# Performance work log

Hardware: AMD Instinct MI355X
Metric: run time of the kernel (lower is better)

The kernel has to match this reference:

```python
import jax, jax.numpy as jnp
import numpy as np

N_NODES = 50000
N_EDGES = 1600000
IN_DIM = 128
HID = 64
N_GRAPHS = 256


def gcn_conv(x, row, col, W, b, n_nodes):
    """PyG GCNConv: symmetric gcn_norm with self-loops, linear-then-aggregate."""
    h = x @ W  # [N, out]
    loop = jnp.arange(n_nodes, dtype=row.dtype)
    r = jnp.concatenate([row, loop])  # sources (messages from x[r])
    c = jnp.concatenate([col, loop])  # targets (aggregate at c)
    ew = jnp.ones(r.shape[0], dtype=x.dtype)
    deg = jax.ops.segment_sum(ew, c, num_segments=n_nodes)
    dinv = jnp.where(deg > 0, jax.lax.rsqrt(deg), 0.0).astype(x.dtype)
    norm = dinv[r] * dinv[c]  # [E+N]
    out = jax.ops.segment_sum(norm[:, None] * h[r], c, num_segments=n_nodes)
    return out + b


def global_mean_pool(x, batch, n_graphs):
    sums = jax.ops.segment_sum(x, batch, num_segments=n_graphs)
    cnt = jax.ops.segment_sum(jnp.ones(x.shape[0], x.dtype), batch, num_segments=n_graphs)
    return sums / jnp.clip(cnt, 1.0)[:, None]


def setup_inputs() -> dict:
    key = jax.random.key(0)
    ks = jax.random.split(key, 12)
    x = jax.random.normal(ks[0], (N_NODES, IN_DIM), dtype=jnp.float32)
    edge_index = jax.random.randint(ks[1], (2, N_EDGES), 0, N_NODES, dtype=jnp.int64)
    batch = jnp.sort(jax.random.randint(ks[2], (N_NODES,), 0, N_GRAPHS, dtype=jnp.int64))
    def glorot(k, shp):
        lim = float(np.sqrt(6.0 / (shp[0] + shp[1])))
        return jax.random.uniform(k, shp, jnp.float32, -lim, lim)
    return {
        "x": x,
        "edge_index": edge_index,
        "batch": batch,
        "W1": glorot(ks[3], (IN_DIM, HID)), "b1": jnp.zeros((HID,), jnp.float32),
        "W2": glorot(ks[4], (HID, HID)), "b2": jnp.zeros((HID,), jnp.float32),
        "W3": glorot(ks[5], (HID, HID)), "b3": jnp.zeros((HID,), jnp.float32),
        "Wl1": glorot(ks[6], (HID, 16)), "bl1": jnp.zeros((16,), jnp.float32),
        "Wl2": glorot(ks[7], (16, 1)), "bl2": jnp.zeros((1,), jnp.float32),
    }


def reference(x, edge_index, batch, W1, b1, W2, b2, W3, b3, Wl1, bl1, Wl2, bl2):
    n = x.shape[0]
    row, col = edge_index[0], edge_index[1]
    h = jax.nn.relu(gcn_conv(x, row, col, W1, b1, n))
    h = jax.nn.relu(gcn_conv(h, row, col, W2, b2, n))
    h = jax.nn.relu(gcn_conv(h, row, col, W3, b3, n))
    g = global_mean_pool(h, batch, N_GRAPHS)  # [G, 64]
    out = (g @ Wl1 + bl1) @ Wl2 + bl2  # [G, 1]
    return out
```

## Files before the change

kernel.cpp:

```cpp
#include <hip/hip_runtime.h>

#define HID 64
#define B1 256
#define NBMAX 200
#define CAP 10368

typedef __attribute__((ext_vector_type(8))) short short8;
typedef __attribute__((ext_vector_type(4))) float float4v;

__device__ __forceinline__ ushort f2bf(float f) {
  unsigned u = __float_as_uint(f);
  unsigned r = (u + 0x7fffu + ((u >> 16) & 1u)) >> 16;
  return (ushort)r;
}
__device__ __forceinline__ float bf2f(ushort v) {
  return __uint_as_float(((unsigned)v) << 16);
}
__device__ __forceinline__ float4 up4(ushort4 v) {
  float4 r;
  r.x = bf2f(v.x);
  r.y = bf2f(v.y);
  r.z = bf2f(v.z);
  r.w = bf2f(v.w);
  return r;
}


__global__ __launch_bounds__(256) void bucket_hist(const int* __restrict__ col, int E, int epb,
                                                   int* __restrict__ buckettot,
                                                   const float* __restrict__ W1,
                                                   const float* __restrict__ W2,
                                                   const float* __restrict__ W3,
                                                   ushort* __restrict__ Wt1h, ushort* __restrict__ Wt1l,
                                                   ushort* __restrict__ Wt2h, ushort* __restrict__ Wt2l,
                                                   ushort* __restrict__ Wt3h, ushort* __restrict__ Wt3l) {
  int b = blockIdx.x, t = threadIdx.x;
  int gt = b * 256 + t;
  if (gt < 128 * 64) {
    int k = gt >> 6, nn = gt & 63;
    float w = W1[gt];
    ushort h = f2bf(w);
    Wt1h[nn * 128 + k] = h;
    Wt1l[nn * 128 + k] = f2bf(w - bf2f(h));
  }
  if (gt < 64 * 64) {
    int k = gt >> 6, nn = gt & 63;
    float w2 = W2[gt], w3 = W3[gt];
    ushort h2 = f2bf(w2), h3 = f2bf(w3);
    Wt2h[nn * 64 + k] = h2;
    Wt2l[nn * 64 + k] = f2bf(w2 - bf2f(h2));
    Wt3h[nn * 64 + k] = h3;
    Wt3l[nn * 64 + k] = f2bf(w3 - bf2f(h3));
  }

  __shared__ int cnt[256];
  cnt[t] = 0;
  __syncthreads();
  int lo = b * epb, hi = min(lo + epb, E);
  for (int e = lo + t; e < hi; e += 256) atomicAdd(&cnt[col[e] >> 8], 1);
  __syncthreads();
  int v = cnt[t];
  if (v > 0) atomicAdd(&buckettot[t], v);
}

__global__ __launch_bounds__(256) void scan_buckettot(const int* __restrict__ buckettot,
                                                      int* __restrict__ bucketbase,
                                                      int* __restrict__ woffglob,
                                                      int* __restrict__ csr_off, int n, int E,
                                                      int nb) {
  __shared__ int s[256];
  int t = threadIdx.x;
  int v = (t < nb) ? buckettot[t] : 0;
  s[t] = v;
  __syncthreads();
  for (int d = 1; d < 256; d <<= 1) {
    int u = (t >= d) ? s[t - d] : 0;
    __syncthreads();
    s[t] += u;
    __syncthreads();
  }
  int base = (t == 0) ? 0 : s[t - 1];
  if (t <= nb) bucketbase[t] = base;
  woffglob[t] = base;
  if (t == 0) csr_off[n] = E;
}

__global__ __launch_bounds__(256) void bin_edges(const int* __restrict__ row,
                                                 const int* __restrict__ col, int E, int epb,
                                                 int* __restrict__ woffglob,
                                                 unsigned* __restrict__ binned) {
  __shared__ int cnt[256];
  __shared__ int ofs[256];
  __shared__ int gb[256];
  __shared__ int lcur[256];
  __shared__ unsigned stage[4096];
  int b = blockIdx.x, t = threadIdx.x;
  int lo = b * epb, hi = min(lo + epb, E);

  for (int bs = lo; bs < hi; bs += 4096) {
    int ecnt = min(4096, hi - bs);
    cnt[t] = 0;
    __syncthreads();
    for (int i = t; i < ecnt; i += 256) atomicAdd(&cnt[col[bs + i] >> 8], 1);
    __syncthreads();
    int v = cnt[t];
    ofs[t] = v;
    __syncthreads();
    for (int d = 1; d < 256; d <<= 1) {
      int u = (t >= d) ? ofs[t - d] : 0;
      __syncthreads();
      ofs[t] += u;
      __syncthreads();
    }
    int excl = ofs[t] - v;
    int g = 0;
    if (v > 0) g = atomicAdd(&woffglob[t], v);
    __syncthreads();
    ofs[t] = excl;
    gb[t] = g;
    lcur[t] = excl;
    __syncthreads();
    for (int i = t; i < ecnt; i += 256) {
      int c = col[bs + i];
      int r = row[bs + i];
      int p = atomicAdd(&lcur[c >> 8], 1);
      stage[p] = ((unsigned)r << 16) | (unsigned)c;
    }
    __syncthreads();
    for (int i = t; i < ecnt; i += 256) {
      unsigned en = stage[i];
      int bb = (en >> 8) & 255;
      binned[gb[bb] + (i - ofs[bb])] = en;
    }
    __syncthreads();
  }
}

__global__ __launch_bounds__(256) void bucket_csr(const unsigned* __restrict__ binned,
                                                  const int* __restrict__ bucketbase,
                                                  int* __restrict__ csr_off,
                                                  int* __restrict__ csr_src,
                                                  float* __restrict__ dinv, int n) {
  __shared__ int lcnt[256];
  __shared__ int lofs[256];
  __shared__ int lsrc[CAP];
  int k = blockIdx.x, t = threadIdx.x;
  int base = bucketbase[k], end = bucketbase[k + 1];
  int s = end - base;
  lcnt[t] = 0;
  __syncthreads();
  for (int i = t; i < s; i += 256) {
    unsigned p = binned[base + i];
    atomicAdd(&lcnt[p & 255u], 1);
  }
  __syncthreads();
  int v = lcnt[t];
  lofs[t] = v;
  __syncthreads();
  for (int d = 1; d < 256; d <<= 1) {
    int u = (t >= d) ? lofs[t - d] : 0;
    __syncthreads();
    lofs[t] += u;
    __syncthreads();
  }
  int excl = lofs[t] - v;
  int node = (k << 8) + t;
  if (node < n) {
    csr_off[node] = base + excl;
    dinv[node] = rsqrtf((float)(v + 1));
  }
  lcnt[t] = excl;
  __syncthreads();
  for (int i = t; i < s; i += 256) {
    unsigned p = binned[base + i];
    int pos = atomicAdd(&lcnt[p & 255u], 1);
    if (pos < CAP) lsrc[pos] = (int)(p >> 16);
  }
  __syncthreads();
  for (int i = t; i < s; i += 256) csr_src[base + i] = (i < CAP) ? lsrc[i] : 0;
}


template <int K>
__global__ __launch_bounds__(256) void gemm_mfma(const float* __restrict__ A,
                                                 const ushort* __restrict__ Wh,
                                                 const ushort* __restrict__ Wl,
                                                 const float* __restrict__ dinv,
                                                 ushort* __restrict__ out, int n) {
  int wave = (blockIdx.x * 256 + threadIdx.x) >> 6;
  int lane = threadIdx.x & 63;
  int row0 = wave * 16;
  if (row0 >= n) return;
  int m = lane & 15;
  int quad = lane >> 4;
  int r = row0 + m;
  int rc = (r < n) ? r : (n - 1);

  float4v acc[4];
#pragma unroll
  for (int t = 0; t < 4; ++t) acc[t] = (float4v){0.f, 0.f, 0.f, 0.f};

#pragma unroll
  for (int k0 = 0; k0 < K; k0 += 32) {
    const float4* xp = (const float4*)&A[(size_t)rc * K + k0 + quad * 8];
    float4 a0 = xp[0];
    float4 a1 = xp[1];
    float av[8] = {a0.x, a0.y, a0.z, a0.w, a1.x, a1.y, a1.z, a1.w};
    short8 ah, al;
#pragma unroll
    for (int i = 0; i < 8; ++i) {
      ushort h = f2bf(av[i]);
      ah[i] = (short)h;
      al[i] = (short)f2bf(av[i] - bf2f(h));
    }
#pragma unroll
    for (int t = 0; t < 4; ++t) {
      size_t wof = (size_t)(t * 16 + m) * K + k0 + quad * 8;
      short8 bh = *(const short8*)&Wh[wof];
      short8 bl = *(const short8*)&Wl[wof];
      acc[t] = __builtin_amdgcn_mfma_f32_16x16x32_bf16(ah, bh, acc[t], 0, 0, 0);
      acc[t] = __builtin_amdgcn_mfma_f32_16x16x32_bf16(al, bh, acc[t], 0, 0, 0);
      acc[t] = __builtin_amdgcn_mfma_f32_16x16x32_bf16(ah, bl, acc[t], 0, 0, 0);
    }
  }

  float4 dv = ((const float4*)dinv)[(row0 >> 2) + quad];
  float dvi[4] = {dv.x, dv.y, dv.z, dv.w};
#pragma unroll
  for (int i = 0; i < 4; ++i) {
    int orow = row0 + quad * 4 + i;
    if (orow < n) {
#pragma unroll
      for (int t = 0; t < 4; ++t) {
        out[(size_t)orow * 64 + t * 16 + m] = f2bf(dvi[i] * acc[t][i]);
      }
    }
  }
}


__global__ __launch_bounds__(256) void agg_kernel(
    const ushort* __restrict__ hs, const int* __restrict__ csr_off,
    const int* __restrict__ csr_src, const float* __restrict__ dinv,
    const float* __restrict__ bias, float* __restrict__ out, int n) {
  int wid = (blockIdx.x * 256 + threadIdx.x) >> 6;
  int lane = threadIdx.x & 63;
  if (wid >= n) return;
  int qe = lane >> 4;
  int fq = lane & 15;
  const ushort4* hs4 = (const ushort4*)hs;

  float4 acc = make_float4(0.f, 0.f, 0.f, 0.f);
  if (qe == 0) {
    float4 s = up4(hs4[(size_t)wid * 16 + fq]);
    acc.x += s.x; acc.y += s.y; acc.z += s.z; acc.w += s.w;
  }

  int j = csr_off[wid];
  int e = csr_off[wid + 1];

  int pre = min(e, (j + 3) & ~3);
  if (j + qe < pre) {
    int s0 = csr_src[j + qe];
    float4 f = up4(hs4[(size_t)s0 * 16 + fq]);
    acc.x += f.x; acc.y += f.y; acc.z += f.z; acc.w += f.w;
  }
  int base = pre;

  for (; base + 16 <= e; base += 16) {
    int4 s = *(const int4*)&csr_src[base + qe * 4];
    float4 f0 = up4(hs4[(size_t)s.x * 16 + fq]);
    float4 f1 = up4(hs4[(size_t)s.y * 16 + fq]);
    float4 f2 = up4(hs4[(size_t)s.z * 16 + fq]);
    float4 f3 = up4(hs4[(size_t)s.w * 16 + fq]);
    acc.x += f0.x + f1.x + f2.x + f3.x;
    acc.y += f0.y + f1.y + f2.y + f3.y;
    acc.z += f0.z + f1.z + f2.z + f3.z;
    acc.w += f0.w + f1.w + f2.w + f3.w;
  }

  for (; base + 4 <= e; base += 4) {
    int s0 = csr_src[base + qe];
    float4 f = up4(hs4[(size_t)s0 * 16 + fq]);
    acc.x += f.x; acc.y += f.y; acc.z += f.z; acc.w += f.w;
  }
  if (base + qe < e) {
    int s0 = csr_src[base + qe];
    float4 f = up4(hs4[(size_t)s0 * 16 + fq]);
    acc.x += f.x; acc.y += f.y; acc.z += f.z; acc.w += f.w;
  }

  acc.x += __shfl_xor(acc.x, 16, 64);
  acc.y += __shfl_xor(acc.y, 16, 64);
  acc.z += __shfl_xor(acc.z, 16, 64);
  acc.w += __shfl_xor(acc.w, 16, 64);
  acc.x += __shfl_xor(acc.x, 32, 64);
  acc.y += __shfl_xor(acc.y, 32, 64);
  acc.z += __shfl_xor(acc.z, 32, 64);
  acc.w += __shfl_xor(acc.w, 32, 64);

  if (qe == 0) {
    float d = dinv[wid];
    float4 bi = ((const float4*)bias)[fq];
    float4 r;
    r.x = fmaxf(d * acc.x + bi.x, 0.f);
    r.y = fmaxf(d * acc.y + bi.y, 0.f);
    r.z = fmaxf(d * acc.z + bi.z, 0.f);
    r.w = fmaxf(d * acc.w + bi.w, 0.f);
    ((float4*)out)[(size_t)wid * 16 + fq] = r;
  }
}


__global__ __launch_bounds__(256) void pool_mlp_kernel(
    const float* __restrict__ a, const int* __restrict__ batch, int n,
    const float* __restrict__ Wl1, const float* __restrict__ bl1,
    const float* __restrict__ Wl2, const float* __restrict__ bl2,
    float* __restrict__ out) {
  int g = blockIdx.x;
  int t = threadIdx.x;
  int lane = t & 63;
  int w = t >> 6;

  int lo = 0, hi = n;
  while (lo < hi) {
    int m = (lo + hi) >> 1;
    if (batch[m] < g) lo = m + 1; else hi = m;
  }
  int start = lo;
  lo = start; hi = n;
  while (lo < hi) {
    int m = (lo + hi) >> 1;
    if (batch[m] < g + 1) lo = m + 1; else hi = m;
  }
  int end = lo;

  float s = 0.f;
  for (int i = start + w; i < end; i += 4) s += a[i * 64 + lane];

  __shared__ float ps[4][64];
  __shared__ float gv[64];
  __shared__ float hv[16];
  ps[w][lane] = s;
  __syncthreads();
  if (w == 0) {
    float tot = ps[0][lane] + ps[1][lane] + ps[2][lane] + ps[3][lane];
    gv[lane] = tot / (float)max(end - start, 1);
  }
  __syncthreads();
  if (t < 16) {
    float h = bl1[t];
    for (int k = 0; k < 64; ++k) h += gv[k] * Wl1[k * 16 + t];
    hv[t] = h;
  }
  __syncthreads();
  if (t == 0) {
    float o = bl2[0];
    for (int j2 = 0; j2 < 16; ++j2) o += hv[j2] * Wl2[j2];
    out[g] = o;
  }
}


extern "C" void kernel_launch(void* const* d_in, const int* in_sizes, int n_in,
                              void* d_out, int out_size, void* d_ws, size_t ws_size,
                              hipStream_t stream) {
  const float* x = (const float*)d_in[0];
  const int* ei = (const int*)d_in[1];
  const int* batch = (const int*)d_in[2];
  const float* W1 = (const float*)d_in[3];
  const float* b1 = (const float*)d_in[4];
  const float* W2 = (const float*)d_in[5];
  const float* b2 = (const float*)d_in[6];
  const float* W3 = (const float*)d_in[7];
  const float* b3 = (const float*)d_in[8];
  const float* Wl1 = (const float*)d_in[9];
  const float* bl1 = (const float*)d_in[10];
  const float* Wl2 = (const float*)d_in[11];
  const float* bl2 = (const float*)d_in[12];

  int n = in_sizes[0] / 128;
  int E = in_sizes[1] / 2;
  int G = out_size;
  int nb = (n + 255) >> 8;
  int epb = (E + B1 - 1) / B1;

  const int* row = ei;
  const int* col = ei + E;

  char* p = (char*)d_ws;
  int* buckettot = (int*)p;   p += 256 * 4;
  int* bucketbase = (int*)p;  p += 272 * 4;
  int* woffglob = (int*)p;    p += 256 * 4;
  int* csr_off = (int*)p;     p += 50064 * 4;
  float* dinv = (float*)p;    p += 50016 * 4;
  ushort* Wt1h = (ushort*)p;  p += 128 * 64 * 2;
  ushort* Wt1l = (ushort*)p;  p += 128 * 64 * 2;
  ushort* Wt2h = (ushort*)p;  p += 64 * 64 * 2;
  ushort* Wt2l = (ushort*)p;  p += 64 * 64 * 2;
  ushort* Wt3h = (ushort*)p;  p += 64 * 64 * 2;
  ushort* Wt3l = (ushort*)p;  p += 64 * 64 * 2;
  int* csr_src = (int*)p;     p += (size_t)((E + 15) / 16 * 16) * 4;
  ushort* hs = (ushort*)p;    p += (size_t)n * 64 * 2;
  float* abuf = (float*)p;
  unsigned* binned = (unsigned*)hs;

  hipMemsetAsync(buckettot, 0, 256 * 4, stream);
  bucket_hist<<<B1, 256, 0, stream>>>(col, E, epb, buckettot,
                                      W1, W2, W3, Wt1h, Wt1l, Wt2h, Wt2l, Wt3h, Wt3l);
  scan_buckettot<<<1, 256, 0, stream>>>(buckettot, bucketbase, woffglob, csr_off, n, E, nb);
  bin_edges<<<B1, 256, 0, stream>>>(row, col, E, epb, woffglob, binned);
  bucket_csr<<<nb, 256, 0, stream>>>(binned, bucketbase, csr_off, csr_src, dinv, n);

  int nwaves = (n + 15) / 16;
  int gblocks = (nwaves + 3) / 4;
  int ablocks = (n * 64 + 255) / 256;

  gemm_mfma<128><<<gblocks, 256, 0, stream>>>(x, Wt1h, Wt1l, dinv, hs, n);
  agg_kernel<<<ablocks, 256, 0, stream>>>(hs, csr_off, csr_src, dinv, b1, abuf, n);
  gemm_mfma<64><<<gblocks, 256, 0, stream>>>(abuf, Wt2h, Wt2l, dinv, hs, n);
  agg_kernel<<<ablocks, 256, 0, stream>>>(hs, csr_off, csr_src, dinv, b2, abuf, n);
  gemm_mfma<64><<<gblocks, 256, 0, stream>>>(abuf, Wt3h, Wt3l, dinv, hs, n);
  agg_kernel<<<ablocks, 256, 0, stream>>>(hs, csr_off, csr_src, dinv, b3, abuf, n);
  pool_mlp_kernel<<<G, 256, 0, stream>>>(abuf, batch, n, Wl1, bl1, Wl2, bl2, (float*)d_out);
}
```

Before: 332.1 us.

## Fuse aggregation with next-layer GEMM and fold mean-pool into final aggregation

Aggregation of layers 1 and 2 now runs inside one kernel with the following MFMA GEMM. Each wave gathers 16 nodes into shared memory, then multiplies them by the next weight matrix, so the fp32 activation buffer no longer goes through global memory. The last aggregation atomically adds into per-graph sums, which replaces the separate pool pass. The bucket histogram writes per-block counts that one kernel then reduces, which removes a memset and the global atomics. In exchange, one wave now handles 16 nodes one after another, which lowers parallelism in the gather phase, and float atomics into 256 graph rows may contend.

```diff
diff --git a/kernel.cpp b/kernel.cpp
--- a/kernel.cpp
+++ b/kernel.cpp
@@ -1,9 +1,7 @@
 #include <hip/hip_runtime.h>
 
-#define HID 64
 #define B1 256
-#define NBMAX 200
-#define CAP 10368
+#define CAP 8960
 
 typedef __attribute__((ext_vector_type(8))) short short8;
 typedef __attribute__((ext_vector_type(4))) float float4v;
@@ -26,16 +24,18 @@
 }
 
 
-__global__ __launch_bounds__(256) void bucket_hist(const int* __restrict__ col, int E, int epb,
-                                                   int* __restrict__ buckettot,
-                                                   const float* __restrict__ W1,
-                                                   const float* __restrict__ W2,
-                                                   const float* __restrict__ W3,
-                                                   ushort* __restrict__ Wt1h, ushort* __restrict__ Wt1l,
-                                                   ushort* __restrict__ Wt2h, ushort* __restrict__ Wt2l,
-                                                   ushort* __restrict__ Wt3h, ushort* __restrict__ Wt3l) {
+__global__ __launch_bounds__(256) void hist_prep(const int* __restrict__ col, int E, int epb,
+                                                 int* __restrict__ blockcnt,
+                                                 float* __restrict__ gsum,
+                                                 const float* __restrict__ W1,
+                                                 const float* __restrict__ W2,
+                                                 const float* __restrict__ W3,
+                                                 ushort* __restrict__ Wt1h, ushort* __restrict__ Wt1l,
+                                                 ushort* __restrict__ Wt2h, ushort* __restrict__ Wt2l,
+                                                 ushort* __restrict__ Wt3h, ushort* __restrict__ Wt3l) {
   int b = blockIdx.x, t = threadIdx.x;
   int gt = b * 256 + t;
+  if (gt < 256 * 64) gsum[gt] = 0.f;
   if (gt < 128 * 64) {
     int k = gt >> 6, nn = gt & 63;
     float w = W1[gt];
@@ -59,18 +59,18 @@
   int lo = b * epb, hi = min(lo + epb, E);
   for (int e = lo + t; e < hi; e += 256) atomicAdd(&cnt[col[e] >> 8], 1);
   __syncthreads();
-  int v = cnt[t];
-  if (v > 0) atomicAdd(&buckettot[t], v);
-}
-
-__global__ __launch_bounds__(256) void scan_buckettot(const int* __restrict__ buckettot,
-                                                      int* __restrict__ bucketbase,
-                                                      int* __restrict__ woffglob,
-                                                      int* __restrict__ csr_off, int n, int E,
-                                                      int nb) {
+  blockcnt[b * 256 + t] = cnt[t];
+}
+
+
+__global__ __launch_bounds__(256) void megascan(const int* __restrict__ blockcnt,
+                                                int* __restrict__ bucketbase,
+                                                int* __restrict__ woffglob,
+                                                int* __restrict__ csr_off, int n, int E, int nb) {
   __shared__ int s[256];
   int t = threadIdx.x;
-  int v = (t < nb) ? buckettot[t] : 0;
+  int v = 0;
+  for (int b = 0; b < 256; ++b) v += blockcnt[b * 256 + t];
   s[t] = v;
   __syncthreads();
   for (int d = 1; d < 256; d <<= 1) {
@@ -84,6 +84,7 @@
   woffglob[t] = base;
   if (t == 0) csr_off[n] = E;
 }
+
 
 __global__ __launch_bounds__(256) void bin_edges(const int* __restrict__ row,
                                                  const int* __restrict__ col, int E, int epb,
@@ -123,8 +124,8 @@
     for (int i = t; i < ecnt; i += 256) {
       int c = col[bs + i];
       int r = row[bs + i];
-      int p = atomicAdd(&lcur[c >> 8], 1);
-      stage[p] = ((unsigned)r << 16) | (unsigned)c;
+      int pos = atomicAdd(&lcur[c >> 8], 1);
+      stage[pos] = ((unsigned)r << 16) | (unsigned)c;
     }
     __syncthreads();
     for (int i = t; i < ecnt; i += 256) {
@@ -135,6 +136,7 @@
     __syncthreads();
   }
 }
+
 
 __global__ __launch_bounds__(256) void bucket_csr(const unsigned* __restrict__ binned,
                                                   const int* __restrict__ bucketbase,
@@ -239,10 +241,144 @@
 }
 
 
-__global__ __launch_bounds__(256) void agg_kernel(
+__global__ __launch_bounds__(256) void layer_fused(
+    const ushort* __restrict__ hsIn, const int* __restrict__ csr_off,
+    const int* __restrict__ csr_src, const float* __restrict__ dinv,
+    const float* __restrict__ bias, const ushort* __restrict__ Wh,
+    const ushort* __restrict__ Wl, ushort* __restrict__ hsOut, int n) {
+  __shared__ float stage[4][16][76];
+  int w = threadIdx.x >> 6;
+  int lane = threadIdx.x & 63;
+  int tile = (blockIdx.x * 256 + threadIdx.x) >> 6;
+  int ntiles = (n + 15) >> 4;
+  if (tile >= ntiles) return;
+  int qe = lane >> 4;
+  int fq = lane & 15;
+  const ushort4* hs4 = (const ushort4*)hsIn;
+
+  for (int m = 0; m < 16; ++m) {
+    int wid = tile * 16 + m;
+    float4 acc = make_float4(0.f, 0.f, 0.f, 0.f);
+    float d = 0.f;
+    if (wid < n) {
+      d = dinv[wid];
+      if (qe == 0) acc = up4(hs4[(size_t)wid * 16 + fq]);
+      int j = csr_off[wid];
+      int e = csr_off[wid + 1];
+      int pre = min(e, (j + 3) & ~3);
+      if (j + qe < pre) {
+        int s0 = csr_src[j + qe];
+        float4 f = up4(hs4[(size_t)s0 * 16 + fq]);
+        acc.x += f.x; acc.y += f.y; acc.z += f.z; acc.w += f.w;
+      }
+      int base = pre;
+      for (; base + 32 <= e; base += 32) {
+        int4 sa = *(const int4*)&csr_src[base + qe * 4];
+        int4 sb = *(const int4*)&csr_src[base + 16 + qe * 4];
+        float4 f0 = up4(hs4[(size_t)sa.x * 16 + fq]);
+        float4 f1 = up4(hs4[(size_t)sa.y * 16 + fq]);
+        float4 f2 = up4(hs4[(size_t)sa.z * 16 + fq]);
+        float4 f3 = up4(hs4[(size_t)sa.w * 16 + fq]);
+        float4 f4 = up4(hs4[(size_t)sb.x * 16 + fq]);
+        float4 f5 = up4(hs4[(size_t)sb.y * 16 + fq]);
+        float4 f6 = up4(hs4[(size_t)sb.z * 16 + fq]);
+        float4 f7 = up4(hs4[(size_t)sb.w * 16 + fq]);
+        acc.x += (f0.x + f1.x) + (f2.x + f3.x) + ((f4.x + f5.x) + (f6.x + f7.x));
+        acc.y += (f0.y + f1.y) + (f2.y + f3.y) + ((f4.y + f5.y) + (f6.y + f7.y));
+        acc.z += (f0.z + f1.z) + (f2.z + f3.z) + ((f4.z + f5.z) + (f6.z + f7.z));
+        acc.w += (f0.w + f1.w) + (f2.w + f3.w) + ((f4.w + f5.w) + (f6.w + f7.w));
+      }
+      for (; base + 16 <= e; base += 16) {
+        int4 s = *(const int4*)&csr_src[base + qe * 4];
+        float4 f0 = up4(hs4[(size_t)s.x * 16 + fq]);
+        float4 f1 = up4(hs4[(size_t)s.y * 16 + fq]);
+        float4 f2 = up4(hs4[(size_t)s.z * 16 + fq]);
+        float4 f3 = up4(hs4[(size_t)s.w * 16 + fq]);
+        acc.x += f0.x + f1.x + f2.x + f3.x;
+        acc.y += f0.y + f1.y + f2.y + f3.y;
+        acc.z += f0.z + f1.z + f2.z + f3.z;
+        acc.w += f0.w + f1.w + f2.w + f3.w;
+      }
+      for (; base + 4 <= e; base += 4) {
+        int s0 = csr_src[base + qe];
+        float4 f = up4(hs4[(size_t)s0 * 16 + fq]);
+        acc.x += f.x; acc.y += f.y; acc.z += f.z; acc.w += f.w;
+      }
+      if (base + qe < e) {
+        int s0 = csr_src[base + qe];
+        float4 f = up4(hs4[(size_t)s0 * 16 + fq]);
+        acc.x += f.x; acc.y += f.y; acc.z += f.z; acc.w += f.w;
+      }
+      acc.x += __shfl_xor(acc.x, 16, 64);
+      acc.y += __shfl_xor(acc.y, 16, 64);
+      acc.z += __shfl_xor(acc.z, 16, 64);
+      acc.w += __shfl_xor(acc.w, 16, 64);
+      acc.x += __shfl_xor(acc.x, 32, 64);
+      acc.y += __shfl_xor(acc.y, 32, 64);
+      acc.z += __shfl_xor(acc.z, 32, 64);
+      acc.w += __shfl_xor(acc.w, 32, 64);
+    }
+    if (qe == 0) {
+      float4 bi = ((const float4*)bias)[fq];
+      float4 r;
+      r.x = fmaxf(d * acc.x + bi.x, 0.f);
+      r.y = fmaxf(d * acc.y + bi.y, 0.f);
+      r.z = fmaxf(d * acc.z + bi.z, 0.f);
+      r.w = fmaxf(d * acc.w + bi.w, 0.f);
+      *(float4*)&stage[w][m][fq * 4] = r;
+    }
+  }
+
+  int m2 = lane & 15;
+  int quad = lane >> 4;
+  float4v acc2[4];
+#pragma unroll
+  for (int t = 0; t < 4; ++t) acc2[t] = (float4v){0.f, 0.f, 0.f, 0.f};
+
+#pragma unroll
+  for (int k0 = 0; k0 < 64; k0 += 32) {
+    float4 a0 = *(const float4*)&stage[w][m2][k0 + quad * 8];
+    float4 a1 = *(const float4*)&stage[w][m2][k0 + quad * 8 + 4];
+    float av[8] = {a0.x, a0.y, a0.z, a0.w, a1.x, a1.y, a1.z, a1.w};
+    short8 ah, al;
+#pragma unroll
+    for (int i = 0; i < 8; ++i) {
+      ushort h = f2bf(av[i]);
+      ah[i] = (short)h;
+      al[i] = (short)f2bf(av[i] - bf2f(h));
+    }
+#pragma unroll
+    for (int t = 0; t < 4; ++t) {
+      size_t wof = (size_t)(t * 16 + m2) * 64 + k0 + quad * 8;
+      short8 bh = *(const short8*)&Wh[wof];
+      short8 bl = *(const short8*)&Wl[wof];
+      acc2[t] = __builtin_amdgcn_mfma_f32_16x16x32_bf16(ah, bh, acc2[t], 0, 0, 0);
+      acc2[t] = __builtin_amdgcn_mfma_f32_16x16x32_bf16(al, bh, acc2[t], 0, 0, 0);
+      acc2[t] = __builtin_amdgcn_mfma_f32_16x16x32_bf16(ah, bl, acc2[t], 0, 0, 0);
+    }
+  }
+
+  int row0 = tile * 16;
+  float4 dv = ((const float4*)dinv)[(row0 >> 2) + quad];
+  float dvi[4] = {dv.x, dv.y, dv.z, dv.w};
+#pragma unroll
+  for (int i = 0; i < 4; ++i) {
+    int orow = row0 + quad * 4 + i;
+    if (orow < n) {
+#pragma unroll
+      for (int t = 0; t < 4; ++t) {
+        hsOut[(size_t)orow * 64 + t * 16 + m2] = f2bf(dvi[i] * acc2[t][i]);
+      }
+    }
+  }
+}
+
+
+__global__ __launch_bounds__(256) void agg_final(
     const ushort* __restrict__ hs, const int* __restrict__ csr_off,
     const int* __restrict__ csr_src, const float* __restrict__ dinv,
-    const float* __restrict__ bias, float* __restrict__ out, int n) {
+    const float* __restrict__ bias, const int* __restrict__ batch,
+    float* __restrict__ gsum, int n) {
   int wid = (blockIdx.x * 256 + threadIdx.x) >> 6;
   int lane = threadIdx.x & 63;
   if (wid >= n) return;
@@ -251,14 +387,10 @@
   const ushort4* hs4 = (const ushort4*)hs;
 
   float4 acc = make_float4(0.f, 0.f, 0.f, 0.f);
-  if (qe == 0) {
-    float4 s = up4(hs4[(size_t)wid * 16 + fq]);
-    acc.x += s.x; acc.y += s.y; acc.z += s.z; acc.w += s.w;
-  }
+  if (qe == 0) acc = up4(hs4[(size_t)wid * 16 + fq]);
 
   int j = csr_off[wid];
   int e = csr_off[wid + 1];
-
   int pre = min(e, (j + 3) & ~3);
   if (j + qe < pre) {
     int s0 = csr_src[j + qe];
@@ -266,7 +398,22 @@
     acc.x += f.x; acc.y += f.y; acc.z += f.z; acc.w += f.w;
   }
   int base = pre;
-
+  for (; base + 32 <= e; base += 32) {
+    int4 sa = *(const int4*)&csr_src[base + qe * 4];
+    int4 sb = *(const int4*)&csr_src[base + 16 + qe * 4];
+    float4 f0 = up4(hs4[(size_t)sa.x * 16 + fq]);
+    float4 f1 = up4(hs4[(size_t)sa.y * 16 + fq]);
+    float4 f2 = up4(hs4[(size_t)sa.z * 16 + fq]);
+    float4 f3 = up4(hs4[(size_t)sa.w * 16 + fq]);
+    float4 f4 = up4(hs4[(size_t)sb.x * 16 + fq]);
+    float4 f5 = up4(hs4[(size_t)sb.y * 16 + fq]);
+    float4 f6 = up4(hs4[(size_t)sb.z * 16 + fq]);
+    float4 f7 = up4(hs4[(size_t)sb.w * 16 + fq]);
+    acc.x += (f0.x + f1.x) + (f2.x + f3.x) + ((f4.x + f5.x) + (f6.x + f7.x));
+    acc.y += (f0.y + f1.y) + (f2.y + f3.y) + ((f4.y + f5.y) + (f6.y + f7.y));
+    acc.z += (f0.z + f1.z) + (f2.z + f3.z) + ((f4.z + f5.z) + (f6.z + f7.z));
+    acc.w += (f0.w + f1.w) + (f2.w + f3.w) + ((f4.w + f5.w) + (f6.w + f7.w));
+  }
   for (; base + 16 <= e; base += 16) {
     int4 s = *(const int4*)&csr_src[base + qe * 4];
     float4 f0 = up4(hs4[(size_t)s.x * 16 + fq]);
@@ -278,7 +425,6 @@
     acc.z += f0.z + f1.z + f2.z + f3.z;
     acc.w += f0.w + f1.w + f2.w + f3.w;
   }
-
   for (; base + 4 <= e; base += 4) {
     int s0 = csr_src[base + qe];
     float4 f = up4(hs4[(size_t)s0 * 16 + fq]);
@@ -307,20 +453,23 @@
     r.y = fmaxf(d * acc.y + bi.y, 0.f);
     r.z = fmaxf(d * acc.z + bi.z, 0.f);
     r.w = fmaxf(d * acc.w + bi.w, 0.f);
-    ((float4*)out)[(size_t)wid * 16 + fq] = r;
-  }
-}
-
-
-__global__ __launch_bounds__(256) void pool_mlp_kernel(
-    const float* __restrict__ a, const int* __restrict__ batch, int n,
+    int g = batch[wid];
+    float* gp = &gsum[(size_t)g * 64 + fq * 4];
+    atomicAdd(gp + 0, r.x);
+    atomicAdd(gp + 1, r.y);
+    atomicAdd(gp + 2, r.z);
+    atomicAdd(gp + 3, r.w);
+  }
+}
+
+
+__global__ __launch_bounds__(64) void mlp_kernel(
+    const float* __restrict__ gsum, const int* __restrict__ batch, int n,
     const float* __restrict__ Wl1, const float* __restrict__ bl1,
     const float* __restrict__ Wl2, const float* __restrict__ bl2,
     float* __restrict__ out) {
   int g = blockIdx.x;
-  int t = threadIdx.x;
-  int lane = t & 63;
-  int w = t >> 6;
+  int lane = threadIdx.x;
 
   int lo = 0, hi = n;
   while (lo < hi) {
@@ -335,26 +484,19 @@
   }
   int end = lo;
 
-  float s = 0.f;
-  for (int i = start + w; i < end; i += 4) s += a[i * 64 + lane];
-
-  __shared__ float ps[4][64];
+  float mean = gsum[(size_t)g * 64 + lane] / (float)max(end - start, 1);
+
   __shared__ float gv[64];
   __shared__ float hv[16];
-  ps[w][lane] = s;
-  __syncthreads();
-  if (w == 0) {
-    float tot = ps[0][lane] + ps[1][lane] + ps[2][lane] + ps[3][lane];
-    gv[lane] = tot / (float)max(end - start, 1);
-  }
-  __syncthreads();
-  if (t < 16) {
-    float h = bl1[t];
-    for (int k = 0; k < 64; ++k) h += gv[k] * Wl1[k * 16 + t];
-    hv[t] = h;
-  }
-  __syncthreads();
-  if (t == 0) {
+  gv[lane] = mean;
+  __syncthreads();
+  if (lane < 16) {
+    float h = bl1[lane];
+    for (int k = 0; k < 64; ++k) h += gv[k] * Wl1[k * 16 + lane];
+    hv[lane] = h;
+  }
+  __syncthreads();
+  if (lane == 0) {
     float o = bl2[0];
     for (int j2 = 0; j2 < 16; ++j2) o += hv[j2] * Wl2[j2];
     out[g] = o;
@@ -389,7 +531,8 @@
   const int* col = ei + E;
 
   char* p = (char*)d_ws;
-  int* buckettot = (int*)p;   p += 256 * 4;
+  int* blockcnt = (int*)p;    p += 256 * 256 * 4;
+  float* gsum = (float*)p;    p += 256 * 64 * 4;
   int* bucketbase = (int*)p;  p += 272 * 4;
   int* woffglob = (int*)p;    p += 256 * 4;
   int* csr_off = (int*)p;     p += 50064 * 4;
@@ -401,26 +544,23 @@
   ushort* Wt3h = (ushort*)p;  p += 64 * 64 * 2;
   ushort* Wt3l = (ushort*)p;  p += 64 * 64 * 2;
   int* csr_src = (int*)p;     p += (size_t)((E + 15) / 16 * 16) * 4;
-  ushort* hs = (ushort*)p;    p += (size_t)n * 64 * 2;
-  float* abuf = (float*)p;
-  unsigned* binned = (unsigned*)hs;
-
-  hipMemsetAsync(buckettot, 0, 256 * 4, stream);
-  bucket_hist<<<B1, 256, 0, stream>>>(col, E, epb, buckettot,
-                                      W1, W2, W3, Wt1h, Wt1l, Wt2h, Wt2l, Wt3h, Wt3l);
-  scan_buckettot<<<1, 256, 0, stream>>>(buckettot, bucketbase, woffglob, csr_off, n, E, nb);
+  ushort* hsA = (ushort*)p;   p += (size_t)n * 64 * 2;
+  ushort* hsB = (ushort*)p;   p += (size_t)n * 64 * 2;
+  unsigned* binned = (unsigned*)hsA;
+
+  hist_prep<<<B1, 256, 0, stream>>>(col, E, epb, blockcnt, gsum,
+                                    W1, W2, W3, Wt1h, Wt1l, Wt2h, Wt2l, Wt3h, Wt3l);
+  megascan<<<1, 256, 0, stream>>>(blockcnt, bucketbase, woffglob, csr_off, n, E, nb);
   bin_edges<<<B1, 256, 0, stream>>>(row, col, E, epb, woffglob, binned);
   bucket_csr<<<nb, 256, 0, stream>>>(binned, bucketbase, csr_off, csr_src, dinv, n);
 
-  int nwaves = (n + 15) / 16;
-  int gblocks = (nwaves + 3) / 4;
+  int ntiles = (n + 15) / 16;
+  int lblocks = (ntiles + 3) / 4;
   int ablocks = (n * 64 + 255) / 256;
 
-  gemm_mfma<128><<<gblocks, 256, 0, stream>>>(x, Wt1h, Wt1l, dinv, hs, n);
-  agg_kernel<<<ablocks, 256, 0, stream>>>(hs, csr_off, csr_src, dinv, b1, abuf, n);
-  gemm_mfma<64><<<gblocks, 256, 0, stream>>>(abuf, Wt2h, Wt2l, dinv, hs, n);
-  agg_kernel<<<ablocks, 256, 0, stream>>>(hs, csr_off, csr_src, dinv, b2, abuf, n);
-  gemm_mfma<64><<<gblocks, 256, 0, stream>>>(abuf, Wt3h, Wt3l, dinv, hs, n);
-  agg_kernel<<<ablocks, 256, 0, stream>>>(hs, csr_off, csr_src, dinv, b3, abuf, n);
-  pool_mlp_kernel<<<G, 256, 0, stream>>>(abuf, batch, n, Wl1, bl1, Wl2, bl2, (float*)d_out);
-}
+  gemm_mfma<128><<<lblocks, 256, 0, stream>>>(x, Wt1h, Wt1l, dinv, hsA, n);
+  layer_fused<<<lblocks, 256, 0, stream>>>(hsA, csr_off, csr_src, dinv, b1, Wt2h, Wt2l, hsB, n);
+  layer_fused<<<lblocks, 256, 0, stream>>>(hsB, csr_off, csr_src, dinv, b2, Wt3h, Wt3l, hsA, n);
+  agg_final<<<ablocks, 256, 0, stream>>>(hsA, csr_off, csr_src, dinv, b3, batch, gsum, n);
+  mlp_kernel<<<G, 64, 0, stream>>>(gsum, batch, n, Wl1, bl1, Wl2, bl2, (float*)d_out);
+}
```

After: 440.0 us. +32.5%, slower.

## Fuse aggregation with next-layer GEMM and replace atomic bucket totals with per-block scan

Applied to the files above, without the earlier changes.

Each block of the new fused kernel gathers 16 nodes' neighbour sums, applies bias, ReLU and normalisation into shared memory, then runs the next layer's split-bf16 MFMA GEMM in place. This removes the fp32 intermediate write and read and two launches per layer, and ping-pongs between two bf16 buffers. The histogram now writes per-block counts that a single-block kernel sums, which drops the memset and global atomics. The gather loop is unrolled to 8 loads per lane with nontemporal index loads, which adds memory-level parallelism at some cost in register pressure.

```diff
diff --git a/kernel.cpp b/kernel.cpp
--- a/kernel.cpp
+++ b/kernel.cpp
@@ -1,12 +1,11 @@
 #include <hip/hip_runtime.h>
 
-#define HID 64
 #define B1 256
-#define NBMAX 200
-#define CAP 10368
+#define CAP 8960
 
 typedef __attribute__((ext_vector_type(8))) short short8;
 typedef __attribute__((ext_vector_type(4))) float float4v;
+typedef __attribute__((ext_vector_type(4))) int int4v;
 
 __device__ __forceinline__ ushort f2bf(float f) {
   unsigned u = __float_as_uint(f);
@@ -26,14 +25,14 @@
 }
 
 
-__global__ __launch_bounds__(256) void bucket_hist(const int* __restrict__ col, int E, int epb,
-                                                   int* __restrict__ buckettot,
-                                                   const float* __restrict__ W1,
-                                                   const float* __restrict__ W2,
-                                                   const float* __restrict__ W3,
-                                                   ushort* __restrict__ Wt1h, ushort* __restrict__ Wt1l,
-                                                   ushort* __restrict__ Wt2h, ushort* __restrict__ Wt2l,
-                                                   ushort* __restrict__ Wt3h, ushort* __restrict__ Wt3l) {
+__global__ __launch_bounds__(256) void hist_prep(const int* __restrict__ col, int E, int epb,
+                                                 int* __restrict__ blockcnt,
+                                                 const float* __restrict__ W1,
+                                                 const float* __restrict__ W2,
+                                                 const float* __restrict__ W3,
+                                                 ushort* __restrict__ Wt1h, ushort* __restrict__ Wt1l,
+                                                 ushort* __restrict__ Wt2h, ushort* __restrict__ Wt2l,
+                                                 ushort* __restrict__ Wt3h, ushort* __restrict__ Wt3l) {
   int b = blockIdx.x, t = threadIdx.x;
   int gt = b * 256 + t;
   if (gt < 128 * 64) {
@@ -59,18 +58,18 @@
   int lo = b * epb, hi = min(lo + epb, E);
   for (int e = lo + t; e < hi; e += 256) atomicAdd(&cnt[col[e] >> 8], 1);
   __syncthreads();
-  int v = cnt[t];
-  if (v > 0) atomicAdd(&buckettot[t], v);
-}
-
-__global__ __launch_bounds__(256) void scan_buckettot(const int* __restrict__ buckettot,
-                                                      int* __restrict__ bucketbase,
-                                                      int* __restrict__ woffglob,
-                                                      int* __restrict__ csr_off, int n, int E,
-                                                      int nb) {
+  blockcnt[b * 256 + t] = cnt[t];
+}
+
+
+__global__ __launch_bounds__(256) void megascan(const int* __restrict__ blockcnt,
+                                                int* __restrict__ bucketbase,
+                                                int* __restrict__ woffglob,
+                                                int* __restrict__ csr_off, int n, int E, int nb) {
   __shared__ int s[256];
   int t = threadIdx.x;
-  int v = (t < nb) ? buckettot[t] : 0;
+  int v = 0;
+  for (int b = 0; b < 256; ++b) v += blockcnt[b * 256 + t];
   s[t] = v;
   __syncthreads();
   for (int d = 1; d < 256; d <<= 1) {
@@ -84,6 +83,7 @@
   woffglob[t] = base;
   if (t == 0) csr_off[n] = E;
 }
+
 
 __global__ __launch_bounds__(256) void bin_edges(const int* __restrict__ row,
                                                  const int* __restrict__ col, int E, int epb,
@@ -123,8 +123,8 @@
     for (int i = t; i < ecnt; i += 256) {
       int c = col[bs + i];
       int r = row[bs + i];
-      int p = atomicAdd(&lcur[c >> 8], 1);
-      stage[p] = ((unsigned)r << 16) | (unsigned)c;
+      int pos = atomicAdd(&lcur[c >> 8], 1);
+      stage[pos] = ((unsigned)r << 16) | (unsigned)c;
     }
     __syncthreads();
     for (int i = t; i < ecnt; i += 256) {
@@ -135,6 +135,7 @@
     __syncthreads();
   }
 }
+
 
 __global__ __launch_bounds__(256) void bucket_csr(const unsigned* __restrict__ binned,
                                                   const int* __restrict__ bucketbase,
@@ -239,7 +240,131 @@
 }
 
 
-__global__ __launch_bounds__(256) void agg_kernel(
+__device__ __forceinline__ float4 gather_node(const ushort4* __restrict__ hs4,
+                                              const int* __restrict__ csr_off,
+                                              const int* __restrict__ csr_src,
+                                              int wid, int qe, int fq) {
+  float4 acc = make_float4(0.f, 0.f, 0.f, 0.f);
+  if (qe == 0) acc = up4(hs4[(size_t)wid * 16 + fq]);
+  int j = csr_off[wid];
+  int e = csr_off[wid + 1];
+  int pre = min(e, (j + 3) & ~3);
+  if (j + qe < pre) {
+    int s0 = csr_src[j + qe];
+    float4 f = up4(hs4[(size_t)s0 * 16 + fq]);
+    acc.x += f.x; acc.y += f.y; acc.z += f.z; acc.w += f.w;
+  }
+  int base = pre;
+  for (; base + 32 <= e; base += 32) {
+    int4v sa = __builtin_nontemporal_load((const int4v*)&csr_src[base + qe * 4]);
+    int4v sb = __builtin_nontemporal_load((const int4v*)&csr_src[base + 16 + qe * 4]);
+    float4 f0 = up4(hs4[(size_t)sa[0] * 16 + fq]);
+    float4 f1 = up4(hs4[(size_t)sa[1] * 16 + fq]);
+    float4 f2 = up4(hs4[(size_t)sa[2] * 16 + fq]);
+    float4 f3 = up4(hs4[(size_t)sa[3] * 16 + fq]);
+    float4 f4 = up4(hs4[(size_t)sb[0] * 16 + fq]);
+    float4 f5 = up4(hs4[(size_t)sb[1] * 16 + fq]);
+    float4 f6 = up4(hs4[(size_t)sb[2] * 16 + fq]);
+    float4 f7 = up4(hs4[(size_t)sb[3] * 16 + fq]);
+    acc.x += (f0.x + f1.x) + (f2.x + f3.x) + ((f4.x + f5.x) + (f6.x + f7.x));
+    acc.y += (f0.y + f1.y) + (f2.y + f3.y) + ((f4.y + f5.y) + (f6.y + f7.y));
+    acc.z += (f0.z + f1.z) + (f2.z + f3.z) + ((f4.z + f5.z) + (f6.z + f7.z));
+    acc.w += (f0.w + f1.w) + (f2.w + f3.w) + ((f4.w + f5.w) + (f6.w + f7.w));
+  }
+  for (; base + 4 <= e; base += 4) {
+    int s0 = csr_src[base + qe];
+    float4 f = up4(hs4[(size_t)s0 * 16 + fq]);
+    acc.x += f.x; acc.y += f.y; acc.z += f.z; acc.w += f.w;
+  }
+  if (base + qe < e) {
+    int s0 = csr_src[base + qe];
+    float4 f = up4(hs4[(size_t)s0 * 16 + fq]);
+    acc.x += f.x; acc.y += f.y; acc.z += f.z; acc.w += f.w;
+  }
+  acc.x += __shfl_xor(acc.x, 16, 64);
+  acc.y += __shfl_xor(acc.y, 16, 64);
+  acc.z += __shfl_xor(acc.z, 16, 64);
+  acc.w += __shfl_xor(acc.w, 16, 64);
+  acc.x += __shfl_xor(acc.x, 32, 64);
+  acc.y += __shfl_xor(acc.y, 32, 64);
+  acc.z += __shfl_xor(acc.z, 32, 64);
+  acc.w += __shfl_xor(acc.w, 32, 64);
+  return acc;
+}
+
+
+__global__ __launch_bounds__(256, 6) void fused_layer(
+    const ushort* __restrict__ hsIn, const int* __restrict__ csr_off,
+    const int* __restrict__ csr_src, const float* __restrict__ dinv,
+    const float* __restrict__ bias, const ushort* __restrict__ Wh,
+    const ushort* __restrict__ Wl, ushort* __restrict__ hsOut, int n) {
+  __shared__ float stage[16][68];
+  int w = threadIdx.x >> 6;
+  int lane = threadIdx.x & 63;
+  int tile = blockIdx.x;
+  int qe = lane >> 4;
+  int fq = lane & 15;
+  const ushort4* hs4 = (const ushort4*)hsIn;
+
+#pragma unroll
+  for (int mi = 0; mi < 4; ++mi) {
+    int m = w * 4 + mi;
+    int wid = tile * 16 + m;
+    float4 acc = make_float4(0.f, 0.f, 0.f, 0.f);
+    float d = 0.f;
+    if (wid < n) {
+      d = dinv[wid];
+      acc = gather_node(hs4, csr_off, csr_src, wid, qe, fq);
+    }
+    if (qe == 0) {
+      float4 bi = ((const float4*)bias)[fq];
+      float4 r;
+      r.x = fmaxf(d * acc.x + bi.x, 0.f);
+      r.y = fmaxf(d * acc.y + bi.y, 0.f);
+      r.z = fmaxf(d * acc.z + bi.z, 0.f);
+      r.w = fmaxf(d * acc.w + bi.w, 0.f);
+      *(float4*)&stage[m][fq * 4] = r;
+    }
+  }
+  __syncthreads();
+
+  int m2 = lane & 15;
+  int quad = lane >> 4;
+  float4v acc2 = (float4v){0.f, 0.f, 0.f, 0.f};
+#pragma unroll
+  for (int k0 = 0; k0 < 64; k0 += 32) {
+    float4 a0 = *(const float4*)&stage[m2][k0 + quad * 8];
+    float4 a1 = *(const float4*)&stage[m2][k0 + quad * 8 + 4];
+    float av[8] = {a0.x, a0.y, a0.z, a0.w, a1.x, a1.y, a1.z, a1.w};
+    short8 ah, al;
+#pragma unroll
+    for (int i = 0; i < 8; ++i) {
+      ushort h = f2bf(av[i]);
+      ah[i] = (short)h;
+      al[i] = (short)f2bf(av[i] - bf2f(h));
+    }
+    size_t wof = (size_t)(w * 16 + m2) * 64 + k0 + quad * 8;
+    short8 bh = *(const short8*)&Wh[wof];
+    short8 bl = *(const short8*)&Wl[wof];
+    acc2 = __builtin_amdgcn_mfma_f32_16x16x32_bf16(ah, bh, acc2, 0, 0, 0);
+    acc2 = __builtin_amdgcn_mfma_f32_16x16x32_bf16(al, bh, acc2, 0, 0, 0);
+    acc2 = __builtin_amdgcn_mfma_f32_16x16x32_bf16(ah, bl, acc2, 0, 0, 0);
+  }
+
+  int row0 = tile * 16;
+  float4 dv = ((const float4*)dinv)[(row0 >> 2) + quad];
+  float dvi[4] = {dv.x, dv.y, dv.z, dv.w};
+#pragma unroll
+  for (int i = 0; i < 4; ++i) {
+    int orow = row0 + quad * 4 + i;
+    if (orow < n) {
+      hsOut[(size_t)orow * 64 + w * 16 + m2] = f2bf(dvi[i] * acc2[i]);
+    }
+  }
+}
+
+
+__global__ __launch_bounds__(256) void agg3_kernel(
     const ushort* __restrict__ hs, const int* __restrict__ csr_off,
     const int* __restrict__ csr_src, const float* __restrict__ dinv,
     const float* __restrict__ bias, float* __restrict__ out, int n) {
@@ -250,57 +375,10 @@
   int fq = lane & 15;
   const ushort4* hs4 = (const ushort4*)hs;
 
-  float4 acc = make_float4(0.f, 0.f, 0.f, 0.f);
+  float d = dinv[wid];
+  float4 acc = gather_node(hs4, csr_off, csr_src, wid, qe, fq);
+
   if (qe == 0) {
-    float4 s = up4(hs4[(size_t)wid * 16 + fq]);
-    acc.x += s.x; acc.y += s.y; acc.z += s.z; acc.w += s.w;
-  }
-
-  int j = csr_off[wid];
-  int e = csr_off[wid + 1];
-
-  int pre = min(e, (j + 3) & ~3);
-  if (j + qe < pre) {
-    int s0 = csr_src[j + qe];
-    float4 f = up4(hs4[(size_t)s0 * 16 + fq]);
-    acc.x += f.x; acc.y += f.y; acc.z += f.z; acc.w += f.w;
-  }
-  int base = pre;
-
-  for (; base + 16 <= e; base += 16) {
-    int4 s = *(const int4*)&csr_src[base + qe * 4];
-    float4 f0 = up4(hs4[(size_t)s.x * 16 + fq]);
-    float4 f1 = up4(hs4[(size_t)s.y * 16 + fq]);
-    float4 f2 = up4(hs4[(size_t)s.z * 16 + fq]);
-    float4 f3 = up4(hs4[(size_t)s.w * 16 + fq]);
-    acc.x += f0.x + f1.x + f2.x + f3.x;
-    acc.y += f0.y + f1.y + f2.y + f3.y;
-    acc.z += f0.z + f1.z + f2.z + f3.z;
-    acc.w += f0.w + f1.w + f2.w + f3.w;
-  }
-
-  for (; base + 4 <= e; base += 4) {
-    int s0 = csr_src[base + qe];
-    float4 f = up4(hs4[(size_t)s0 * 16 + fq]);
-    acc.x += f.x; acc.y += f.y; acc.z += f.z; acc.w += f.w;
-  }
-  if (base + qe < e) {
-    int s0 = csr_src[base + qe];
-    float4 f = up4(hs4[(size_t)s0 * 16 + fq]);
-    acc.x += f.x; acc.y += f.y; acc.z += f.z; acc.w += f.w;
-  }
-
-  acc.x += __shfl_xor(acc.x, 16, 64);
-  acc.y += __shfl_xor(acc.y, 16, 64);
-  acc.z += __shfl_xor(acc.z, 16, 64);
-  acc.w += __shfl_xor(acc.w, 16, 64);
-  acc.x += __shfl_xor(acc.x, 32, 64);
-  acc.y += __shfl_xor(acc.y, 32, 64);
-  acc.z += __shfl_xor(acc.z, 32, 64);
-  acc.w += __shfl_xor(acc.w, 32, 64);
-
-  if (qe == 0) {
-    float d = dinv[wid];
     float4 bi = ((const float4*)bias)[fq];
     float4 r;
     r.x = fmaxf(d * acc.x + bi.x, 0.f);
@@ -389,7 +467,7 @@
   const int* col = ei + E;
 
   char* p = (char*)d_ws;
-  int* buckettot = (int*)p;   p += 256 * 4;
+  int* blockcnt = (int*)p;    p += 256 * 256 * 4;
   int* bucketbase = (int*)p;  p += 272 * 4;
   int* woffglob = (int*)p;    p += 256 * 4;
   int* csr_off = (int*)p;     p += 50064 * 4;
@@ -401,26 +479,24 @@
   ushort* Wt3h = (ushort*)p;  p += 64 * 64 * 2;
   ushort* Wt3l = (ushort*)p;  p += 64 * 64 * 2;
   int* csr_src = (int*)p;     p += (size_t)((E + 15) / 16 * 16) * 4;
-  ushort* hs = (ushort*)p;    p += (size_t)n * 64 * 2;
+  ushort* hsA = (ushort*)p;   p += (size_t)n * 64 * 2;
+  ushort* hsB = (ushort*)p;   p += (size_t)n * 64 * 2;
   float* abuf = (float*)p;
-  unsigned* binned = (unsigned*)hs;
-
-  hipMemsetAsync(buckettot, 0, 256 * 4, stream);
-  bucket_hist<<<B1, 256, 0, stream>>>(col, E, epb, buckettot,
-                                      W1, W2, W3, Wt1h, Wt1l, Wt2h, Wt2l, Wt3h, Wt3l);
-  scan_buckettot<<<1, 256, 0, stream>>>(buckettot, bucketbase, woffglob, csr_off, n, E, nb);
+  unsigned* binned = (unsigned*)hsA;
+
+  hist_prep<<<B1, 256, 0, stream>>>(col, E, epb, blockcnt,
+                                    W1, W2, W3, Wt1h, Wt1l, Wt2h, Wt2l, Wt3h, Wt3l);
+  megascan<<<1, 256, 0, stream>>>(blockcnt, bucketbase, woffglob, csr_off, n, E, nb);
   bin_edges<<<B1, 256, 0, stream>>>(row, col, E, epb, woffglob, binned);
   bucket_csr<<<nb, 256, 0, stream>>>(binned, bucketbase, csr_off, csr_src, dinv, n);
 
-  int nwaves = (n + 15) / 16;
-  int gblocks = (nwaves + 3) / 4;
+  int ntiles = (n + 15) / 16;
+  int gblocks = (ntiles + 3) / 4;
   int ablocks = (n * 64 + 255) / 256;
 
-  gemm_mfma<128><<<gblocks, 256, 0, stream>>>(x, Wt1h, Wt1l, dinv, hs, n);
-  agg_kernel<<<ablocks, 256, 0, stream>>>(hs, csr_off, csr_src, dinv, b1, abuf, n);
-  gemm_mfma<64><<<gblocks, 256, 0, stream>>>(abuf, Wt2h, Wt2l, dinv, hs, n);
-  agg_kernel<<<ablocks, 256, 0, stream>>>(hs, csr_off, csr_src, dinv, b2, abuf, n);
-  gemm_mfma<64><<<gblocks, 256, 0, stream>>>(abuf, Wt3h, Wt3l, dinv, hs, n);
-  agg_kernel<<<ablocks, 256, 0, stream>>>(hs, csr_off, csr_src, dinv, b3, abuf, n);
+  gemm_mfma<128><<<gblocks, 256, 0, stream>>>(x, Wt1h, Wt1l, dinv, hsA, n);
+  fused_layer<<<ntiles, 256, 0, stream>>>(hsA, csr_off, csr_src, dinv, b1, Wt2h, Wt2l, hsB, n);
+  fused_layer<<<ntiles, 256, 0, stream>>>(hsB, csr_off, csr_src, dinv, b2, Wt3h, Wt3l, hsA, n);
+  agg3_kernel<<<ablocks, 256, 0, stream>>>(hsA, csr_off, csr_src, dinv, b3, abuf, n);
   pool_mlp_kernel<<<G, 256, 0, stream>>>(abuf, batch, n, Wl1, bl1, Wl2, bl2, (float*)d_out);
 }
```

After: 357.0 us. +7.5%, slower.
